# Optimization experiments

Hardware: AMD Instinct MI355X
Metric: run time of the kernel (lower is better)

Reference implementation:

```python
import jax, jax.numpy as jnp
import numpy as np

D = 512      # d_model
H = 8        # nhead
HD = D // H  # head dim
L = 8        # axis-0 length (torch seq dim, batch_first=False)
S = 128      # axis-1 length (torch batch dim; relation-tensor axis)
NL = 3       # encoder layers
EPS = 1e-5


def setup_inputs() -> dict:
    key = jax.random.key(0)
    ks = jax.random.split(key, 16)
    w = lambda k, shape: jax.random.normal(k, shape, jnp.float32) * 0.02
    return {
        "x": jax.random.normal(ks[0], (L, S, D), jnp.float32),
        # stacked per-layer transformer params (leading dim = NL)
        "attn_in_w": w(ks[1], (NL, 3 * D, D)), "attn_in_b": jnp.zeros((NL, 3 * D), jnp.float32),
        "attn_out_w": w(ks[2], (NL, D, D)),    "attn_out_b": jnp.zeros((NL, D), jnp.float32),
        "ln1_w": jnp.ones((NL, D), jnp.float32), "ln1_b": jnp.zeros((NL, D), jnp.float32),
        "ln2_w": jnp.ones((NL, D), jnp.float32), "ln2_b": jnp.zeros((NL, D), jnp.float32),
        "ff1_w": w(ks[3], (NL, 4 * D, D)), "ff1_b": jnp.zeros((NL, 4 * D), jnp.float32),
        "ff2_w": w(ks[4], (NL, D, 4 * D)), "ff2_b": jnp.zeros((NL, D), jnp.float32),
        "fln_w": jnp.ones((D,), jnp.float32), "fln_b": jnp.zeros((D,), jnp.float32),
        # 4 projection MLPs stacked: 0=sub, 1=obj, 2=verb_sub, 3=verb_obj
        "mlp_w0": w(ks[5], (4, D, D)), "mlp_b0": jnp.zeros((4, D), jnp.float32),
        "mlp_w1": w(ks[6], (4, D, D)), "mlp_b1": jnp.zeros((4, D), jnp.float32),
        "mlp_w2": w(ks[7], (4, D, D)), "mlp_b2": jnp.zeros((4, D), jnp.float32),
    }


def _ln(x, w, b):
    m = jnp.mean(x, axis=-1, keepdims=True)
    v = jnp.mean(jnp.square(x - m), axis=-1, keepdims=True)
    return (x - m) * jax.lax.rsqrt(v + EPS) * w + b


def _mha(x, in_w, in_b, out_w, out_b):
    # x: (L, B, D); attention over axis 0 (torch batch_first=False semantics)
    l, b, _ = x.shape
    qkv = x @ in_w.T + in_b                      # (L, B, 3D)
    q, k, v = jnp.split(qkv, 3, axis=-1)
    q = q.reshape(l, b, H, HD)
    k = k.reshape(l, b, H, HD)
    v = v.reshape(l, b, H, HD)
    scores = jnp.einsum("lbhd,mbhd->bhlm", q, k) / jnp.sqrt(jnp.float32(HD))
    attn = jax.nn.softmax(scores, axis=-1)
    o = jnp.einsum("bhlm,mbhd->lbhd", attn, v).reshape(l, b, D)
    return o @ out_w.T + out_b


def _mlp(x, w0, b0, w1, b1, w2, b2):
    h = jax.nn.relu(x @ w0.T + b0)
    h = jax.nn.relu(h @ w1.T + b1)
    return h @ w2.T + b2


def _forward(x, attn_in_w, attn_in_b, attn_out_w, attn_out_b,
             ln1_w, ln1_b, ln2_w, ln2_b, ff1_w, ff1_b, ff2_w, ff2_b,
             fln_w, fln_b, mlp_w0, mlp_b0, mlp_w1, mlp_b1, mlp_w2, mlp_b2):
    # TransformerEncoder (post-norm, relu, no dropout at eval)
    h = x
    for i in range(NL):
        h = _ln(h + _mha(h, attn_in_w[i], attn_in_b[i], attn_out_w[i], attn_out_b[i]),
                ln1_w[i], ln1_b[i])
        ff = jax.nn.relu(h @ ff1_w[i].T + ff1_b[i]) @ ff2_w[i].T + ff2_b[i]
        h = _ln(h + ff, ln2_w[i], ln2_b[i])
    h = _ln(h, fln_w, fln_b)  # final encoder norm

    sub = _mlp(h, mlp_w0[0], mlp_b0[0], mlp_w1[0], mlp_b1[0], mlp_w2[0], mlp_b2[0])
    obj = _mlp(h, mlp_w0[1], mlp_b0[1], mlp_w1[1], mlp_b1[1], mlp_w2[1], mlp_b2[1])
    vsub = _mlp(h, mlp_w0[2], mlp_b0[2], mlp_w1[2], mlp_b1[2], mlp_w2[2], mlp_b2[2])
    vobj = _mlp(h, mlp_w0[3], mlp_b0[3], mlp_w1[3], mlp_b1[3], mlp_w2[3], mlp_b2[3])

    # sub.unsqueeze(1) * vsub.unsqueeze(2): (B0, S, S, D)
    sub4 = sub[:, None, :, :] * vsub[:, :, None, :]
    obj4 = obj[:, None, :, :] * vobj[:, :, None, :]
    # p_x = sub4 @ obj4.transpose(-2, -1): (B0, S, S, S)
    return jnp.einsum("bijd,bikd->bijk", sub4, obj4)


def reference(x, attn_in_w, attn_in_b, attn_out_w, attn_out_b,
              ln1_w, ln1_b, ln2_w, ln2_b, ff1_w, ff1_b, ff2_w, ff2_b,
              fln_w, fln_b, mlp_w0, mlp_b0, mlp_w1, mlp_b1, mlp_w2, mlp_b2):
    return _forward(x, attn_in_w, attn_in_b, attn_out_w, attn_out_b,
                    ln1_w, ln1_b, ln2_w, ln2_b, ff1_w, ff1_b, ff2_w, ff2_b,
                    fln_w, fln_b, mlp_w0, mlp_b0, mlp_w1, mlp_b1, mlp_w2, mlp_b2)
```

## Files before the change

kernel.cpp:

```cpp
#include <hip/hip_runtime.h>
#include <hip/hip_bf16.h>

#define DEV __device__ __forceinline__

typedef __attribute__((ext_vector_type(8))) short bf16x8;
typedef __attribute__((ext_vector_type(8))) unsigned short u16x8;
typedef __attribute__((ext_vector_type(4))) float f32x4;

DEV unsigned short f2bf(float f) {
  return __builtin_bit_cast(unsigned short, __float2bfloat16(f));
}
DEV float bf2f(unsigned short h) { return __uint_as_float(((unsigned int)h) << 16); }

DEV int swz(int row, int byteoff) { return row * 128 + (byteoff ^ ((row & 7) << 4)); }

struct CvtJobs { const float* s[8]; unsigned short* d[8]; int n[8]; };
__global__ void cvtw_kernel(CvtJobs J) {
  const int seg = blockIdx.y;
  const float* __restrict__ src = J.s[seg];
  unsigned short* __restrict__ dst = J.d[seg];
  const int n = J.n[seg];
  long i = ((long)blockIdx.x * blockDim.x + threadIdx.x) * 8;
  long stride = (long)gridDim.x * blockDim.x * 8;
  for (; i < n; i += stride) {
    f32x4 a = *(const f32x4*)(src + i);
    f32x4 b = *(const f32x4*)(src + i + 4);
    u16x8 o;
    o[0] = f2bf(a[0]); o[1] = f2bf(a[1]); o[2] = f2bf(a[2]); o[3] = f2bf(a[3]);
    o[4] = f2bf(b[0]); o[5] = f2bf(b[1]); o[6] = f2bf(b[2]); o[7] = f2bf(b[3]);
    *(u16x8*)(dst + i) = o;
  }
}

template <int BM, int BN, int ALN, int RES, int RLN, int ACT, int STATS, int OUTF32, int OUTBF>
__global__ __launch_bounds__(256) void gemm2_kernel(
    const unsigned short* __restrict__ Xb, const float* __restrict__ Xf,
    const float* __restrict__ sA, const float* __restrict__ gA, const float* __restrict__ bA,
    const unsigned short* __restrict__ W, const float* __restrict__ bias,
    const float* __restrict__ resf, const float* __restrict__ sR,
    const float* __restrict__ gR, const float* __restrict__ bR,
    float* __restrict__ Yf, unsigned short* __restrict__ Ybf, float* __restrict__ stats,
    int M, int N, int K, long xbs, long wbs, long bbs, long ybs) {
  constexpr int CA = BM / 32, CB = BN / 32;
  constexpr int ABY = BM * 64 * 2, BBY = BN * 64 * 2;
  constexpr int MI = BM / 32, NI = BN / 32;
  __shared__ __align__(16) char Asb[2 * ABY];
  __shared__ __align__(16) char Bsb[2 * BBY];
  const int t = threadIdx.x;
  const int bn = blockIdx.x, bm = blockIdx.y, bz = blockIdx.z;
  const int lane = t & 63, wv = t >> 6, wr = wv >> 1, wc = wv & 1;

  int rowA[CA], slotA[CA], rowB[CB], slotB[CB];
#pragma unroll
  for (int c = 0; c < CA; ++c) { int id = c * 256 + t; rowA[c] = id >> 3; slotA[c] = id & 7; }
#pragma unroll
  for (int c = 0; c < CB; ++c) { int id = c * 256 + t; rowB[c] = id >> 3; slotB[c] = id & 7; }

  float mA[CA], iA[CA];
  if (ALN) {
#pragma unroll
    for (int c = 0; c < CA; ++c) {
      const int gm = bm * BM + rowA[c];
      const float s = sA[2 * gm], q = sA[2 * gm + 1];
      mA[c] = s * (1.f / 512.f);
      iA[c] = rsqrtf(q * (1.f / 512.f) - mA[c] * mA[c] + 1e-5f);
    }
  }

  f32x4 acc[MI][NI];
#pragma unroll
  for (int mi = 0; mi < MI; ++mi)
#pragma unroll
    for (int ni = 0; ni < NI; ++ni) acc[mi][ni] = f32x4{0.f, 0.f, 0.f, 0.f};

  u16x8 ra[CA], rb[CB];
  f32x4 raf[CA][2];
  auto load = [&](int kt) {
#pragma unroll
    for (int c = 0; c < CA; ++c) {
      if (ALN) {
        const float* p = Xf + (long)(bm * BM + rowA[c]) * K + kt + slotA[c] * 8;
        raf[c][0] = *(const f32x4*)p;
        raf[c][1] = *(const f32x4*)(p + 4);
      } else {
        ra[c] = *(const u16x8*)(Xb + (long)bz * xbs + (long)(bm * BM + rowA[c]) * K + kt + slotA[c] * 8);
      }
    }
#pragma unroll
    for (int c = 0; c < CB; ++c)
      rb[c] = *(const u16x8*)(W + (long)bz * wbs + (long)(bn * BN + rowB[c]) * K + kt + slotB[c] * 8);
  };
  auto store = [&](int cur, int kt) {
#pragma unroll
    for (int c = 0; c < CA; ++c) {
      if (ALN) {
        const int col = kt + slotA[c] * 8;
        f32x4 g0 = *(const f32x4*)(gA + col), g1 = *(const f32x4*)(gA + col + 4);
        f32x4 b0 = *(const f32x4*)(bA + col), b1 = *(const f32x4*)(bA + col + 4);
        u16x8 o;
#pragma unroll
        for (int j = 0; j < 4; ++j) o[j] = f2bf((raf[c][0][j] - mA[c]) * iA[c] * g0[j] + b0[j]);
#pragma unroll
        for (int j = 0; j < 4; ++j) o[4 + j] = f2bf((raf[c][1][j] - mA[c]) * iA[c] * g1[j] + b1[j]);
        *(u16x8*)(Asb + cur * ABY + swz(rowA[c], slotA[c] * 16)) = o;
      } else {
        *(u16x8*)(Asb + cur * ABY + swz(rowA[c], slotA[c] * 16)) = ra[c];
      }
    }
#pragma unroll
    for (int c = 0; c < CB; ++c)
      *(u16x8*)(Bsb + cur * BBY + swz(rowB[c], slotB[c] * 16)) = rb[c];
  };

  const int NT = K >> 6;
  load(0);
  store(0, 0);
  load(64);
  __syncthreads();
  for (int ki = 0; ki < NT; ++ki) {
    const int cur = ki & 1;
    if (ki + 1 < NT) store(cur ^ 1, (ki + 1) << 6);
    if (ki + 2 < NT) load((ki + 2) << 6);
#pragma unroll
    for (int kk = 0; kk < 2; ++kk) {
      const int kb = kk * 64 + ((lane >> 4) << 4);
      bf16x8 af[MI], bfv[NI];
#pragma unroll
      for (int mi = 0; mi < MI; ++mi)
        af[mi] = *(const bf16x8*)(Asb + cur * ABY + swz(wr * (BM / 2) + mi * 16 + (lane & 15), kb));
#pragma unroll
      for (int ni = 0; ni < NI; ++ni)
        bfv[ni] = *(const bf16x8*)(Bsb + cur * BBY + swz(wc * (BN / 2) + ni * 16 + (lane & 15), kb));
#pragma unroll
      for (int mi = 0; mi < MI; ++mi)
#pragma unroll
        for (int ni = 0; ni < NI; ++ni)
          acc[mi][ni] = __builtin_amdgcn_mfma_f32_16x16x32_bf16(af[mi], bfv[ni], acc[mi][ni], 0, 0, 0);
    }
    __syncthreads();
  }

#pragma unroll
  for (int mi = 0; mi < MI; ++mi) {
#pragma unroll
    for (int rr = 0; rr < 4; ++rr) {
      const int gm = bm * BM + wr * (BM / 2) + mi * 16 + ((lane >> 4) << 2) + rr;
      float mR, iR;
      if (RES && RLN) {
        const float s = sR[2 * gm], q = sR[2 * gm + 1];
        mR = s * (1.f / 512.f);
        iR = rsqrtf(q * (1.f / 512.f) - mR * mR + 1e-5f);
      }
      float srow = 0.f, qrow = 0.f;
#pragma unroll
      for (int ni = 0; ni < NI; ++ni) {
        const int gn = bn * BN + wc * (BN / 2) + ni * 16 + (lane & 15);
        float v = acc[mi][ni][rr] + bias[(long)bz * bbs + gn];
        if (RES) {
          float r = resf[(long)gm * 512 + gn];
          if (RLN) r = (r - mR) * iR * gR[gn] + bR[gn];
          v += r;
        }
        if (ACT) v = fmaxf(v, 0.f);
        if (STATS) { srow += v; qrow += v * v; }
        const long o = (long)bz * ybs + (long)gm * N + gn;
        if (OUTF32) Yf[o] = v;
        if (OUTBF) Ybf[o] = f2bf(v);
      }
      if (STATS) {
#pragma unroll
        for (int msk = 1; msk < 16; msk <<= 1) {
          srow += __shfl_xor(srow, msk, 64);
          qrow += __shfl_xor(qrow, msk, 64);
        }
        if ((lane & 15) == 0) {
          atomicAdd(&stats[2 * gm], srow);
          atomicAdd(&stats[2 * gm + 1], qrow);
        }
      }
    }
  }
}

__global__ __launch_bounds__(256) void attn_kernel(const unsigned short* __restrict__ qkv,
                                                   unsigned short* __restrict__ o) {
  __shared__ float P[512];
  const int s = blockIdx.x;
  const int t = threadIdx.x;
#pragma unroll
  for (int rep = 0; rep < 2; ++rep) {
    const int idx = t + rep * 256;
    const int h = idx >> 6, l = (idx >> 3) & 7, m = idx & 7;
    const unsigned short* qp = qkv + (long)(l * 128 + s) * 1536 + h * 64;
    const unsigned short* kp = qkv + (long)(m * 128 + s) * 1536 + 512 + h * 64;
    float acc = 0.f;
#pragma unroll
    for (int c = 0; c < 64; c += 8) {
      u16x8 q8 = *(const u16x8*)(qp + c);
      u16x8 k8 = *(const u16x8*)(kp + c);
#pragma unroll
      for (int j = 0; j < 8; ++j) acc += bf2f(q8[j]) * bf2f(k8[j]);
    }
    P[idx] = acc * 0.125f;
  }
  __syncthreads();
  if (t < 64) {
    const int base = t * 8;
    float mx = -1e30f;
#pragma unroll
    for (int m = 0; m < 8; ++m) mx = fmaxf(mx, P[base + m]);
    float e[8], sum = 0.f;
#pragma unroll
    for (int m = 0; m < 8; ++m) { e[m] = expf(P[base + m] - mx); sum += e[m]; }
    const float inv = 1.f / sum;
#pragma unroll
    for (int m = 0; m < 8; ++m) P[base + m] = e[m] * inv;
  }
  __syncthreads();
#pragma unroll
  for (int rep = 0; rep < 16; ++rep) {
    const int idx = t + rep * 256;
    const int d = idx & 63, h = (idx >> 6) & 7, l = idx >> 9;
    float acc = 0.f;
#pragma unroll
    for (int m = 0; m < 8; ++m)
      acc += P[h * 64 + l * 8 + m] * bf2f(qkv[(long)(m * 128 + s) * 1536 + 1024 + h * 64 + d]);
    o[(long)(l * 128 + s) * 512 + h * 64 + d] = f2bf(acc);
  }
}

__global__ __launch_bounds__(256) void lastln_kernel(const float* __restrict__ t2,
                                                     const float* __restrict__ S,
                                                     const float* __restrict__ g2,
                                                     const float* __restrict__ b2,
                                                     const float* __restrict__ gf,
                                                     const float* __restrict__ bf_,
                                                     unsigned short* __restrict__ out) {
  const int t = threadIdx.x, lane = t & 63, wv = t >> 6;
  const int row = blockIdx.x * 4 + wv;
  const float* p = t2 + (long)row * 512 + lane * 8;
  f32x4 a = *(const f32x4*)p;
  f32x4 c = *(const f32x4*)(p + 4);
  const float s0 = S[2 * row], q0 = S[2 * row + 1];
  const float m1 = s0 * (1.f / 512.f);
  const float i1 = rsqrtf(q0 * (1.f / 512.f) - m1 * m1 + 1e-5f);
  float v[8];
  const float* g2p = g2 + lane * 8;
  const float* b2p = b2 + lane * 8;
#pragma unroll
  for (int j = 0; j < 4; ++j) v[j] = (a[j] - m1) * i1 * g2p[j] + b2p[j];
#pragma unroll
  for (int j = 0; j < 4; ++j) v[4 + j] = (c[j] - m1) * i1 * g2p[4 + j] + b2p[4 + j];
  float s = 0.f, q = 0.f;
#pragma unroll
  for (int j = 0; j < 8; ++j) { s += v[j]; q += v[j] * v[j]; }
#pragma unroll
  for (int msk = 32; msk; msk >>= 1) { s += __shfl_xor(s, msk, 64); q += __shfl_xor(q, msk, 64); }
  const float m2 = s * (1.f / 512.f);
  const float i2 = rsqrtf(q * (1.f / 512.f) - m2 * m2 + 1e-5f);
  const float* gfp = gf + lane * 8;
  const float* bfp = bf_ + lane * 8;
  u16x8 o;
#pragma unroll
  for (int j = 0; j < 8; ++j) o[j] = f2bf((v[j] - m2) * i2 * gfp[j] + bfp[j]);
  *(u16x8*)(out + (long)row * 512 + lane * 8) = o;
}

__global__ __launch_bounds__(256) void phasec_kernel(const float* __restrict__ subp,
                                                     const unsigned short* __restrict__ objbf,
                                                     const float* __restrict__ vsub,
                                                     const float* __restrict__ vobj,
                                                     float* __restrict__ out) {
  constexpr int ABY = 128 * 64 * 2;
  __shared__ __align__(16) char SMEM[67584];
  char* Asb = SMEM;
  char* Bsb = SMEM + 2 * ABY;
  float* Wl = (float*)(SMEM + 4 * ABY);
  const int t = threadIdx.x;
  const int i = blockIdx.x, b = blockIdx.y;
  const long base_bi = ((long)b * 128 + i) * 512;
  for (int d = t; d < 512; d += 256) Wl[d] = vsub[base_bi + d] * vobj[base_bi + d];

  const int lane = t & 63, wv = t >> 6;
  const int wr = wv >> 1, wc = wv & 1;
  f32x4 acc[4][4] = {};

  int row[4], slot[4];
#pragma unroll
  for (int c = 0; c < 4; ++c) { int id = c * 256 + t; row[c] = id >> 3; slot[c] = id & 7; }

  f32x4 fa[4][2];
  u16x8 rb[4];
  auto load = [&](int kt) {
#pragma unroll
    for (int c = 0; c < 4; ++c) {
      const long g = ((long)b * 128 + row[c]) * 512 + kt + slot[c] * 8;
      fa[c][0] = *(const f32x4*)(subp + g);
      fa[c][1] = *(const f32x4*)(subp + g + 4);
      rb[c] = *(const u16x8*)(objbf + g);
    }
  };
  auto store = [&](int cur, int ktd) {
#pragma unroll
    for (int c = 0; c < 4; ++c) {
      const float* wp = Wl + ktd + slot[c] * 8;
      f32x4 w0 = *(const f32x4*)wp;
      f32x4 w1 = *(const f32x4*)(wp + 4);
      u16x8 oa;
      oa[0] = f2bf(fa[c][0][0] * w0[0]); oa[1] = f2bf(fa[c][0][1] * w0[1]);
      oa[2] = f2bf(fa[c][0][2] * w0[2]); oa[3] = f2bf(fa[c][0][3] * w0[3]);
      oa[4] = f2bf(fa[c][1][0] * w1[0]); oa[5] = f2bf(fa[c][1][1] * w1[1]);
      oa[6] = f2bf(fa[c][1][2] * w1[2]); oa[7] = f2bf(fa[c][1][3] * w1[3]);
      *(u16x8*)(Asb + cur * ABY + swz(row[c], slot[c] * 16)) = oa;
      *(u16x8*)(Bsb + cur * ABY + swz(row[c], slot[c] * 16)) = rb[c];
    }
  };

  __syncthreads();
  load(0);
  store(0, 0);
  load(64);
  __syncthreads();
  for (int ki = 0; ki < 8; ++ki) {
    const int cur = ki & 1;
    if (ki + 1 < 8) store(cur ^ 1, (ki + 1) * 64);
    if (ki + 2 < 8) load((ki + 2) * 64);
#pragma unroll
    for (int kk = 0; kk < 2; ++kk) {
      const int kb = kk * 64 + ((lane >> 4) << 4);
      bf16x8 af[4], bfv[4];
#pragma unroll
      for (int mi = 0; mi < 4; ++mi)
        af[mi] = *(const bf16x8*)(Asb + cur * ABY + swz(wr * 64 + mi * 16 + (lane & 15), kb));
#pragma unroll
      for (int ni = 0; ni < 4; ++ni)
        bfv[ni] = *(const bf16x8*)(Bsb + cur * ABY + swz(wc * 64 + ni * 16 + (lane & 15), kb));
#pragma unroll
      for (int mi = 0; mi < 4; ++mi)
#pragma unroll
        for (int ni = 0; ni < 4; ++ni)
          acc[mi][ni] = __builtin_amdgcn_mfma_f32_16x16x32_bf16(af[mi], bfv[ni], acc[mi][ni], 0, 0, 0);
    }
    __syncthreads();
  }
  float* C = (float*)SMEM;
#pragma unroll
  for (int mi = 0; mi < 4; ++mi)
#pragma unroll
    for (int rr = 0; rr < 4; ++rr) {
      const int j = wr * 64 + mi * 16 + ((lane >> 4) << 2) + rr;
      float* crow = C + j * 132 + wc * 64 + (lane & 15);
#pragma unroll
      for (int ni = 0; ni < 4; ++ni) crow[ni * 16] = acc[mi][ni][rr];
    }
  __syncthreads();
  float* ob = out + ((long)b * 128 + i) * 128 * 128;
  const int cc = (t & 31) * 4, jb = (t >> 5) * 16;
#pragma unroll
  for (int q = 0; q < 16; ++q) {
    const int j = jb + q;
    f32x4 v = *(const f32x4*)(C + j * 132 + cc);
    *(f32x4*)(ob + (long)j * 128 + cc) = v;
  }
}

extern "C" void kernel_launch(void* const* d_in, const int* in_sizes, int n_in, void* d_out,
                              int out_size, void* d_ws, size_t ws_size, hipStream_t stream) {
  const float* x          = (const float*)d_in[0];
  const float* attn_in_w  = (const float*)d_in[1];
  const float* attn_in_b  = (const float*)d_in[2];
  const float* attn_out_w = (const float*)d_in[3];
  const float* attn_out_b = (const float*)d_in[4];
  const float* ln1_w = (const float*)d_in[5];
  const float* ln1_b = (const float*)d_in[6];
  const float* ln2_w = (const float*)d_in[7];
  const float* ln2_b = (const float*)d_in[8];
  const float* ff1_w = (const float*)d_in[9];
  const float* ff1_b = (const float*)d_in[10];
  const float* ff2_w = (const float*)d_in[11];
  const float* ff2_b = (const float*)d_in[12];
  const float* fln_w = (const float*)d_in[13];
  const float* fln_b = (const float*)d_in[14];
  const float* mlp_w0 = (const float*)d_in[15];
  const float* mlp_b0 = (const float*)d_in[16];
  const float* mlp_w1 = (const float*)d_in[17];
  const float* mlp_b1 = (const float*)d_in[18];
  const float* mlp_w2 = (const float*)d_in[19];
  const float* mlp_b2 = (const float*)d_in[20];
  float* out = (float*)d_out;
  (void)in_sizes; (void)n_in; (void)out_size; (void)ws_size;

  char* ws = (char*)d_ws;
  size_t off = 0;
  auto alloc = [&](size_t bytes) -> void* {
    void* p = (void*)(ws + off);
    off += (bytes + 255) & ~(size_t)255;
    return p;
  };
  float* stats        = (float*)alloc((size_t)6 * 1024 * 2 * 4);
  unsigned short* wq  = (unsigned short*)alloc((size_t)3 * 1536 * 512 * 2);
  unsigned short* wo  = (unsigned short*)alloc((size_t)3 * 512 * 512 * 2);
  unsigned short* wf1 = (unsigned short*)alloc((size_t)3 * 2048 * 512 * 2);
  unsigned short* wf2 = (unsigned short*)alloc((size_t)3 * 512 * 2048 * 2);
  unsigned short* wm0 = (unsigned short*)alloc((size_t)4 * 512 * 512 * 2);
  unsigned short* wm1 = (unsigned short*)alloc((size_t)4 * 512 * 512 * 2);
  unsigned short* wm2 = (unsigned short*)alloc((size_t)4 * 512 * 512 * 2);
  unsigned short* hbf0 = (unsigned short*)alloc((size_t)1024 * 512 * 2);
  unsigned short* t1  = (unsigned short*)alloc((size_t)1024 * 2048 * 2);
  unsigned short* ao  = (unsigned short*)alloc((size_t)1024 * 512 * 2);
  float* t2a          = (float*)alloc((size_t)1024 * 512 * 4);
  float* t2b          = (float*)alloc((size_t)1024 * 512 * 4);
  unsigned short* hbfH = (unsigned short*)alloc((size_t)1024 * 512 * 2);
  unsigned short* z1  = (unsigned short*)alloc((size_t)4 * 1024 * 512 * 2);
  unsigned short* z2  = (unsigned short*)alloc((size_t)4 * 1024 * 512 * 2);
  float* hf4          = (float*)alloc((size_t)4 * 1024 * 512 * 4);
  unsigned short* hb4 = (unsigned short*)alloc((size_t)4 * 1024 * 512 * 2);

  hipMemsetAsync(stats, 0, (size_t)6 * 1024 * 2 * 4, stream);

  CvtJobs J;
  J.s[0] = attn_in_w;  J.d[0] = wq;  J.n[0] = 3 * 1536 * 512;
  J.s[1] = attn_out_w; J.d[1] = wo;  J.n[1] = 3 * 512 * 512;
  J.s[2] = ff1_w;      J.d[2] = wf1; J.n[2] = 3 * 2048 * 512;
  J.s[3] = ff2_w;      J.d[3] = wf2; J.n[3] = 3 * 512 * 2048;
  J.s[4] = mlp_w0;     J.d[4] = wm0; J.n[4] = 4 * 512 * 512;
  J.s[5] = mlp_w1;     J.d[5] = wm1; J.n[5] = 4 * 512 * 512;
  J.s[6] = mlp_w2;     J.d[6] = wm2; J.n[6] = 4 * 512 * 512;
  J.s[7] = x;          J.d[7] = hbf0; J.n[7] = 1024 * 512;
  cvtw_kernel<<<dim3(512, 8), 256, 0, stream>>>(J);

  for (int L = 0; L < 3; ++L) {
    float* Sout = stats + (2 * L) * 2048;
    float* Sff  = stats + (2 * L + 1) * 2048;
    const float* Sprev = stats + (2 * L - 1) * 2048;
    if (L == 0)
      gemm2_kernel<64, 128, 0, 0, 0, 0, 0, 0, 1><<<dim3(12, 16), 256, 0, stream>>>(
          hbf0, nullptr, nullptr, nullptr, nullptr, wq, attn_in_b, nullptr, nullptr, nullptr,
          nullptr, nullptr, t1, nullptr, 1024, 1536, 512, 0, 0, 0, 0);
    else
      gemm2_kernel<64, 128, 1, 0, 0, 0, 0, 0, 1><<<dim3(12, 16), 256, 0, stream>>>(
          nullptr, t2b, Sprev, ln2_w + (L - 1) * 512, ln2_b + (L - 1) * 512,
          wq + (long)L * 1536 * 512, attn_in_b + L * 1536, nullptr, nullptr, nullptr,
          nullptr, nullptr, t1, nullptr, 1024, 1536, 512, 0, 0, 0, 0);
    attn_kernel<<<128, 256, 0, stream>>>(t1, ao);
    if (L == 0)
      gemm2_kernel<32, 64, 0, 1, 0, 0, 1, 1, 0><<<dim3(8, 32), 256, 0, stream>>>(
          ao, nullptr, nullptr, nullptr, nullptr, wo, attn_out_b, x, nullptr, nullptr, nullptr,
          t2a, nullptr, Sout, 1024, 512, 512, 0, 0, 0, 0);
    else
      gemm2_kernel<32, 64, 0, 1, 1, 0, 1, 1, 0><<<dim3(8, 32), 256, 0, stream>>>(
          ao, nullptr, nullptr, nullptr, nullptr, wo + (long)L * 512 * 512, attn_out_b + L * 512,
          t2b, Sprev, ln2_w + (L - 1) * 512, ln2_b + (L - 1) * 512,
          t2a, nullptr, Sout, 1024, 512, 512, 0, 0, 0, 0);
    gemm2_kernel<64, 128, 1, 0, 0, 1, 0, 0, 1><<<dim3(16, 16), 256, 0, stream>>>(
        nullptr, t2a, Sout, ln1_w + L * 512, ln1_b + L * 512,
        wf1 + (long)L * 2048 * 512, ff1_b + L * 2048, nullptr, nullptr, nullptr, nullptr,
        nullptr, t1, nullptr, 1024, 2048, 512, 0, 0, 0, 0);
    gemm2_kernel<32, 64, 0, 1, 1, 0, 1, 1, 0><<<dim3(8, 32), 256, 0, stream>>>(
        t1, nullptr, nullptr, nullptr, nullptr, wf2 + (long)L * 512 * 2048, ff2_b + L * 512,
        t2a, Sout, ln1_w + L * 512, ln1_b + L * 512,
        t2b, nullptr, Sff, 1024, 512, 2048, 0, 0, 0, 0);
  }
  lastln_kernel<<<256, 256, 0, stream>>>(t2b, stats + 5 * 2048, ln2_w + 2 * 512, ln2_b + 2 * 512,
                                         fln_w, fln_b, hbfH);
  gemm2_kernel<64, 128, 0, 0, 0, 1, 0, 0, 1><<<dim3(4, 16, 4), 256, 0, stream>>>(
      hbfH, nullptr, nullptr, nullptr, nullptr, wm0, mlp_b0, nullptr, nullptr, nullptr, nullptr,
      nullptr, z1, nullptr, 1024, 512, 512, 0, 512 * 512, 512, 1024 * 512);
  gemm2_kernel<64, 128, 0, 0, 0, 1, 0, 0, 1><<<dim3(4, 16, 4), 256, 0, stream>>>(
      z1, nullptr, nullptr, nullptr, nullptr, wm1, mlp_b1, nullptr, nullptr, nullptr, nullptr,
      nullptr, z2, nullptr, 1024, 512, 512, 1024 * 512, 512 * 512, 512, 1024 * 512);
  gemm2_kernel<64, 128, 0, 0, 0, 0, 0, 1, 1><<<dim3(4, 16, 4), 256, 0, stream>>>(
      z2, nullptr, nullptr, nullptr, nullptr, wm2, mlp_b2, nullptr, nullptr, nullptr, nullptr,
      hf4, hb4, nullptr, 1024, 512, 512, 1024 * 512, 512 * 512, 512, 1024 * 512);

  phasec_kernel<<<dim3(128, 8), 256, 0, stream>>>(
      hf4, hb4 + 1 * 1024 * 512, hf4 + 2L * 1024 * 512, hf4 + 3L * 1024 * 512, out);
}
```

Baseline: 388.8 us.

## Drop weight pre-conversion kernel and fuse attention with output projection

Removes the separate fp32-to-bf16 conversion pass over all weights and the input. GEMMs now load fp32 weights (and fp32 x in layer 0) and convert them while staging into shared memory. The attention kernel is merged with the output projection, residual add and LayerNorm statistics into one 512-thread kernel per sequence column. This saves a launch and a global round trip of the attention output, at the cost of reading fp32 weights in every GEMM tile and giving the fused kernel only 128 blocks with each block sweeping the full 512x512 output weight.

Measured after the change: 412.3 us. 6.1% more time.

```diff
diff --git a/kernel.cpp b/kernel.cpp
--- a/kernel.cpp
+++ b/kernel.cpp
@@ -14,29 +14,13 @@
 
 DEV int swz(int row, int byteoff) { return row * 128 + (byteoff ^ ((row & 7) << 4)); }
 
-struct CvtJobs { const float* s[8]; unsigned short* d[8]; int n[8]; };
-__global__ void cvtw_kernel(CvtJobs J) {
-  const int seg = blockIdx.y;
-  const float* __restrict__ src = J.s[seg];
-  unsigned short* __restrict__ dst = J.d[seg];
-  const int n = J.n[seg];
-  long i = ((long)blockIdx.x * blockDim.x + threadIdx.x) * 8;
-  long stride = (long)gridDim.x * blockDim.x * 8;
-  for (; i < n; i += stride) {
-    f32x4 a = *(const f32x4*)(src + i);
-    f32x4 b = *(const f32x4*)(src + i + 4);
-    u16x8 o;
-    o[0] = f2bf(a[0]); o[1] = f2bf(a[1]); o[2] = f2bf(a[2]); o[3] = f2bf(a[3]);
-    o[4] = f2bf(b[0]); o[5] = f2bf(b[1]); o[6] = f2bf(b[2]); o[7] = f2bf(b[3]);
-    *(u16x8*)(dst + i) = o;
-  }
-}
-
-template <int BM, int BN, int ALN, int RES, int RLN, int ACT, int STATS, int OUTF32, int OUTBF>
+template <int BM, int BN, int ALN, int AF32, int WF32, int RES, int RLN, int ACT, int STATS,
+          int OUTF32, int OUTBF>
 __global__ __launch_bounds__(256) void gemm2_kernel(
     const unsigned short* __restrict__ Xb, const float* __restrict__ Xf,
     const float* __restrict__ sA, const float* __restrict__ gA, const float* __restrict__ bA,
-    const unsigned short* __restrict__ W, const float* __restrict__ bias,
+    const unsigned short* __restrict__ Wb, const float* __restrict__ Wf,
+    const float* __restrict__ bias,
     const float* __restrict__ resf, const float* __restrict__ sR,
     const float* __restrict__ gR, const float* __restrict__ bR,
     float* __restrict__ Yf, unsigned short* __restrict__ Ybf, float* __restrict__ stats,
@@ -74,11 +58,11 @@
     for (int ni = 0; ni < NI; ++ni) acc[mi][ni] = f32x4{0.f, 0.f, 0.f, 0.f};
 
   u16x8 ra[CA], rb[CB];
-  f32x4 raf[CA][2];
+  f32x4 raf[CA][2], rbf[CB][2];
   auto load = [&](int kt) {
 #pragma unroll
     for (int c = 0; c < CA; ++c) {
-      if (ALN) {
+      if (ALN || AF32) {
         const float* p = Xf + (long)(bm * BM + rowA[c]) * K + kt + slotA[c] * 8;
         raf[c][0] = *(const f32x4*)p;
         raf[c][1] = *(const f32x4*)(p + 4);
@@ -87,29 +71,51 @@
       }
     }
 #pragma unroll
-    for (int c = 0; c < CB; ++c)
-      rb[c] = *(const u16x8*)(W + (long)bz * wbs + (long)(bn * BN + rowB[c]) * K + kt + slotB[c] * 8);
+    for (int c = 0; c < CB; ++c) {
+      if (WF32) {
+        const float* p = Wf + (long)bz * wbs + (long)(bn * BN + rowB[c]) * K + kt + slotB[c] * 8;
+        rbf[c][0] = *(const f32x4*)p;
+        rbf[c][1] = *(const f32x4*)(p + 4);
+      } else {
+        rb[c] = *(const u16x8*)(Wb + (long)bz * wbs + (long)(bn * BN + rowB[c]) * K + kt + slotB[c] * 8);
+      }
+    }
   };
   auto store = [&](int cur, int kt) {
 #pragma unroll
     for (int c = 0; c < CA; ++c) {
+      u16x8 o;
       if (ALN) {
         const int col = kt + slotA[c] * 8;
         f32x4 g0 = *(const f32x4*)(gA + col), g1 = *(const f32x4*)(gA + col + 4);
         f32x4 b0 = *(const f32x4*)(bA + col), b1 = *(const f32x4*)(bA + col + 4);
-        u16x8 o;
 #pragma unroll
         for (int j = 0; j < 4; ++j) o[j] = f2bf((raf[c][0][j] - mA[c]) * iA[c] * g0[j] + b0[j]);
 #pragma unroll
         for (int j = 0; j < 4; ++j) o[4 + j] = f2bf((raf[c][1][j] - mA[c]) * iA[c] * g1[j] + b1[j]);
-        *(u16x8*)(Asb + cur * ABY + swz(rowA[c], slotA[c] * 16)) = o;
+      } else if (AF32) {
+#pragma unroll
+        for (int j = 0; j < 4; ++j) o[j] = f2bf(raf[c][0][j]);
+#pragma unroll
+        for (int j = 0; j < 4; ++j) o[4 + j] = f2bf(raf[c][1][j]);
       } else {
-        *(u16x8*)(Asb + cur * ABY + swz(rowA[c], slotA[c] * 16)) = ra[c];
-      }
-    }
-#pragma unroll
-    for (int c = 0; c < CB; ++c)
-      *(u16x8*)(Bsb + cur * BBY + swz(rowB[c], slotB[c] * 16)) = rb[c];
+        o = ra[c];
+      }
+      *(u16x8*)(Asb + cur * ABY + swz(rowA[c], slotA[c] * 16)) = o;
+    }
+#pragma unroll
+    for (int c = 0; c < CB; ++c) {
+      u16x8 o;
+      if (WF32) {
+#pragma unroll
+        for (int j = 0; j < 4; ++j) o[j] = f2bf(rbf[c][0][j]);
+#pragma unroll
+        for (int j = 0; j < 4; ++j) o[4 + j] = f2bf(rbf[c][1][j]);
+      } else {
+        o = rb[c];
+      }
+      *(u16x8*)(Bsb + cur * BBY + swz(rowB[c], slotB[c] * 16)) = o;
+    }
   };
 
   const int NT = K >> 6;
@@ -182,15 +188,50 @@
   }
 }
 
-__global__ __launch_bounds__(256) void attn_kernel(const unsigned short* __restrict__ qkv,
-                                                   unsigned short* __restrict__ o) {
+template <int RLN>
+__global__ __launch_bounds__(512) void attnop_kernel(
+    const unsigned short* __restrict__ qkv, const float* __restrict__ Wf,
+    const float* __restrict__ bias, const float* __restrict__ resf,
+    const float* __restrict__ sR, const float* __restrict__ gR, const float* __restrict__ bR,
+    float* __restrict__ t2a, float* __restrict__ stats) {
   __shared__ float P[512];
+  __shared__ float Sred[8][16][2];
+  __shared__ __align__(16) char As[16 * 1024];
+  __shared__ __align__(16) char Bs[2 * 128 * 128];
   const int s = blockIdx.x;
   const int t = threadIdx.x;
-#pragma unroll
-  for (int rep = 0; rep < 2; ++rep) {
-    const int idx = t + rep * 256;
-    const int h = idx >> 6, l = (idx >> 3) & 7, m = idx & 7;
+  const int lane = t & 63, w = t >> 6;
+
+  int rowB[2], slotB[2];
+#pragma unroll
+  for (int c = 0; c < 2; ++c) { int id = c * 512 + t; rowB[c] = id >> 3; slotB[c] = id & 7; }
+  f32x4 rbf[2][2];
+  auto loadB = [&](int tau) {
+    const int nb = (tau >> 3) * 128, kt = (tau & 7) * 64;
+#pragma unroll
+    for (int c = 0; c < 2; ++c) {
+      const float* p = Wf + (long)(nb + rowB[c]) * 512 + kt + slotB[c] * 8;
+      rbf[c][0] = *(const f32x4*)p;
+      rbf[c][1] = *(const f32x4*)(p + 4);
+    }
+  };
+  auto storeB = [&](int cur) {
+#pragma unroll
+    for (int c = 0; c < 2; ++c) {
+      u16x8 o;
+#pragma unroll
+      for (int j = 0; j < 4; ++j) o[j] = f2bf(rbf[c][0][j]);
+#pragma unroll
+      for (int j = 0; j < 4; ++j) o[4 + j] = f2bf(rbf[c][1][j]);
+      *(u16x8*)(Bs + cur * 16384 + swz(rowB[c], slotB[c] * 16)) = o;
+    }
+  };
+  loadB(0);
+
+  *(f32x4*)(As + 8 * 1024 + t * 16) = f32x4{0.f, 0.f, 0.f, 0.f};
+
+  {
+    const int h = t >> 6, l = (t >> 3) & 7, m = t & 7;
     const unsigned short* qp = qkv + (long)(l * 128 + s) * 1536 + h * 64;
     const unsigned short* kp = qkv + (long)(m * 128 + s) * 1536 + 512 + h * 64;
     float acc = 0.f;
@@ -201,7 +242,7 @@
 #pragma unroll
       for (int j = 0; j < 8; ++j) acc += bf2f(q8[j]) * bf2f(k8[j]);
     }
-    P[idx] = acc * 0.125f;
+    P[t] = acc * 0.125f;
   }
   __syncthreads();
   if (t < 64) {
@@ -217,15 +258,82 @@
     for (int m = 0; m < 8; ++m) P[base + m] = e[m] * inv;
   }
   __syncthreads();
-#pragma unroll
-  for (int rep = 0; rep < 16; ++rep) {
-    const int idx = t + rep * 256;
-    const int d = idx & 63, h = (idx >> 6) & 7, l = idx >> 9;
-    float acc = 0.f;
-#pragma unroll
-    for (int m = 0; m < 8; ++m)
-      acc += P[h * 64 + l * 8 + m] * bf2f(qkv[(long)(m * 128 + s) * 1536 + 1024 + h * 64 + d]);
-    o[(long)(l * 128 + s) * 512 + h * 64 + d] = f2bf(acc);
+  {
+    const int l = t >> 6, c0 = lane * 8, h = c0 >> 6;
+    float o[8] = {0.f, 0.f, 0.f, 0.f, 0.f, 0.f, 0.f, 0.f};
+#pragma unroll
+    for (int m = 0; m < 8; ++m) {
+      const float p = P[h * 64 + l * 8 + m];
+      u16x8 v8 = *(const u16x8*)(qkv + (long)(m * 128 + s) * 1536 + 1024 + c0);
+#pragma unroll
+      for (int j = 0; j < 8; ++j) o[j] += p * bf2f(v8[j]);
+    }
+    u16x8 pk;
+#pragma unroll
+    for (int j = 0; j < 8; ++j) pk[j] = f2bf(o[j]);
+    *(u16x8*)(As + l * 1024 + ((c0 * 2) ^ ((l & 7) << 4))) = pk;
+  }
+  __syncthreads();
+
+  f32x4 acc[4] = {};
+  storeB(0);
+  loadB(1);
+  __syncthreads();
+  for (int tau = 0; tau < 32; ++tau) {
+    const int cur = tau & 1;
+    if (tau + 1 < 32) storeB(cur ^ 1);
+    if (tau + 2 < 32) loadB(tau + 2);
+    const int nc = tau >> 3;
+#pragma unroll
+    for (int kk = 0; kk < 2; ++kk) {
+      const int arow = lane & 15;
+      const int kbyte = ((tau & 7) << 7) + (kk << 6) + ((lane >> 4) << 4);
+      bf16x8 af = *(const bf16x8*)(As + arow * 1024 + (kbyte ^ ((arow & 7) << 4)));
+      bf16x8 bv = *(const bf16x8*)(Bs + cur * 16384 +
+                                   swz(w * 16 + (lane & 15), (kk << 6) + ((lane >> 4) << 4)));
+      acc[nc] = __builtin_amdgcn_mfma_f32_16x16x32_bf16(af, bv, acc[nc], 0, 0, 0);
+    }
+    __syncthreads();
+  }
+
+#pragma unroll
+  for (int rr = 0; rr < 4; ++rr) {
+    const int l = ((lane >> 4) << 2) + rr;
+    if (l < 8) {
+      const int g = l * 128 + s;
+      float mR, iR;
+      if (RLN) {
+        const float sv = sR[2 * g], qv = sR[2 * g + 1];
+        mR = sv * (1.f / 512.f);
+        iR = rsqrtf(qv * (1.f / 512.f) - mR * mR + 1e-5f);
+      }
+      float sr = 0.f, qr = 0.f;
+#pragma unroll
+      for (int nc = 0; nc < 4; ++nc) {
+        const int n = nc * 128 + w * 16 + (lane & 15);
+        float v = acc[nc][rr] + bias[n];
+        float r = resf[(long)g * 512 + n];
+        if (RLN) r = (r - mR) * iR * gR[n] + bR[n];
+        v += r;
+        sr += v; qr += v * v;
+        t2a[(long)g * 512 + n] = v;
+      }
+#pragma unroll
+      for (int msk = 1; msk < 16; msk <<= 1) {
+        sr += __shfl_xor(sr, msk, 64);
+        qr += __shfl_xor(qr, msk, 64);
+      }
+      if ((lane & 15) == 0) { Sred[w][l][0] = sr; Sred[w][l][1] = qr; }
+    }
+  }
+  __syncthreads();
+  if (t < 8) {
+    float S = 0.f, Q = 0.f;
+#pragma unroll
+    for (int ww = 0; ww < 8; ++ww) { S += Sred[ww][t][0]; Q += Sred[ww][t][1]; }
+    const int g = t * 128 + s;
+    stats[2 * g] = S;
+    stats[2 * g + 1] = Q;
   }
 }
 
@@ -397,81 +505,65 @@
     off += (bytes + 255) & ~(size_t)255;
     return p;
   };
-  float* stats        = (float*)alloc((size_t)6 * 1024 * 2 * 4);
-  unsigned short* wq  = (unsigned short*)alloc((size_t)3 * 1536 * 512 * 2);
-  unsigned short* wo  = (unsigned short*)alloc((size_t)3 * 512 * 512 * 2);
-  unsigned short* wf1 = (unsigned short*)alloc((size_t)3 * 2048 * 512 * 2);
-  unsigned short* wf2 = (unsigned short*)alloc((size_t)3 * 512 * 2048 * 2);
-  unsigned short* wm0 = (unsigned short*)alloc((size_t)4 * 512 * 512 * 2);
-  unsigned short* wm1 = (unsigned short*)alloc((size_t)4 * 512 * 512 * 2);
-  unsigned short* wm2 = (unsigned short*)alloc((size_t)4 * 512 * 512 * 2);
-  unsigned short* hbf0 = (unsigned short*)alloc((size_t)1024 * 512 * 2);
-  unsigned short* t1  = (unsigned short*)alloc((size_t)1024 * 2048 * 2);
-  unsigned short* ao  = (unsigned short*)alloc((size_t)1024 * 512 * 2);
-  float* t2a          = (float*)alloc((size_t)1024 * 512 * 4);
-  float* t2b          = (float*)alloc((size_t)1024 * 512 * 4);
+  float* stats         = (float*)alloc((size_t)6 * 1024 * 2 * 4);
+  unsigned short* t1   = (unsigned short*)alloc((size_t)1024 * 2048 * 2);
+  float* t2a           = (float*)alloc((size_t)1024 * 512 * 4);
+  float* t2b           = (float*)alloc((size_t)1024 * 512 * 4);
   unsigned short* hbfH = (unsigned short*)alloc((size_t)1024 * 512 * 2);
-  unsigned short* z1  = (unsigned short*)alloc((size_t)4 * 1024 * 512 * 2);
-  unsigned short* z2  = (unsigned short*)alloc((size_t)4 * 1024 * 512 * 2);
-  float* hf4          = (float*)alloc((size_t)4 * 1024 * 512 * 4);
-  unsigned short* hb4 = (unsigned short*)alloc((size_t)4 * 1024 * 512 * 2);
+  unsigned short* z1   = (unsigned short*)alloc((size_t)4 * 1024 * 512 * 2);
+  unsigned short* z2   = (unsigned short*)alloc((size_t)4 * 1024 * 512 * 2);
+  float* hf4           = (float*)alloc((size_t)4 * 1024 * 512 * 4);
+  unsigned short* hb4  = (unsigned short*)alloc((size_t)4 * 1024 * 512 * 2);
 
   hipMemsetAsync(stats, 0, (size_t)6 * 1024 * 2 * 4, stream);
-
-  CvtJobs J;
-  J.s[0] = attn_in_w;  J.d[0] = wq;  J.n[0] = 3 * 1536 * 512;
-  J.s[1] = attn_out_w; J.d[1] = wo;  J.n[1] = 3 * 512 * 512;
-  J.s[2] = ff1_w;      J.d[2] = wf1; J.n[2] = 3 * 2048 * 512;
-  J.s[3] = ff2_w;      J.d[3] = wf2; J.n[3] = 3 * 512 * 2048;
-  J.s[4] = mlp_w0;     J.d[4] = wm0; J.n[4] = 4 * 512 * 512;
-  J.s[5] = mlp_w1;     J.d[5] = wm1; J.n[5] = 4 * 512 * 512;
-  J.s[6] = mlp_w2;     J.d[6] = wm2; J.n[6] = 4 * 512 * 512;
-  J.s[7] = x;          J.d[7] = hbf0; J.n[7] = 1024 * 512;
-  cvtw_kernel<<<dim3(512, 8), 256, 0, stream>>>(J);
 
   for (int L = 0; L < 3; ++L) {
     float* Sout = stats + (2 * L) * 2048;
     float* Sff  = stats + (2 * L + 1) * 2048;
     const float* Sprev = stats + (2 * L - 1) * 2048;
     if (L == 0)
-      gemm2_kernel<64, 128, 0, 0, 0, 0, 0, 0, 1><<<dim3(12, 16), 256, 0, stream>>>(
-          hbf0, nullptr, nullptr, nullptr, nullptr, wq, attn_in_b, nullptr, nullptr, nullptr,
-          nullptr, nullptr, t1, nullptr, 1024, 1536, 512, 0, 0, 0, 0);
+      gemm2_kernel<64, 128, 0, 1, 1, 0, 0, 0, 0, 0, 1><<<dim3(12, 16), 256, 0, stream>>>(
+          nullptr, x, nullptr, nullptr, nullptr, nullptr, attn_in_w, attn_in_b,
+          nullptr, nullptr, nullptr, nullptr, nullptr, t1, nullptr,
+          1024, 1536, 512, 0, 0, 0, 0);
     else
-      gemm2_kernel<64, 128, 1, 0, 0, 0, 0, 0, 1><<<dim3(12, 16), 256, 0, stream>>>(
+      gemm2_kernel<64, 128, 1, 0, 1, 0, 0, 0, 0, 0, 1><<<dim3(12, 16), 256, 0, stream>>>(
           nullptr, t2b, Sprev, ln2_w + (L - 1) * 512, ln2_b + (L - 1) * 512,
-          wq + (long)L * 1536 * 512, attn_in_b + L * 1536, nullptr, nullptr, nullptr,
-          nullptr, nullptr, t1, nullptr, 1024, 1536, 512, 0, 0, 0, 0);
-    attn_kernel<<<128, 256, 0, stream>>>(t1, ao);
+          nullptr, attn_in_w + (long)L * 1536 * 512, attn_in_b + L * 1536,
+          nullptr, nullptr, nullptr, nullptr, nullptr, t1, nullptr,
+          1024, 1536, 512, 0, 0, 0, 0);
     if (L == 0)
-      gemm2_kernel<32, 64, 0, 1, 0, 0, 1, 1, 0><<<dim3(8, 32), 256, 0, stream>>>(
-          ao, nullptr, nullptr, nullptr, nullptr, wo, attn_out_b, x, nullptr, nullptr, nullptr,
-          t2a, nullptr, Sout, 1024, 512, 512, 0, 0, 0, 0);
+      attnop_kernel<0><<<128, 512, 0, stream>>>(
+          t1, attn_out_w, attn_out_b, x, nullptr, nullptr, nullptr, t2a, Sout);
     else
-      gemm2_kernel<32, 64, 0, 1, 1, 0, 1, 1, 0><<<dim3(8, 32), 256, 0, stream>>>(
-          ao, nullptr, nullptr, nullptr, nullptr, wo + (long)L * 512 * 512, attn_out_b + L * 512,
-          t2b, Sprev, ln2_w + (L - 1) * 512, ln2_b + (L - 1) * 512,
-          t2a, nullptr, Sout, 1024, 512, 512, 0, 0, 0, 0);
-    gemm2_kernel<64, 128, 1, 0, 0, 1, 0, 0, 1><<<dim3(16, 16), 256, 0, stream>>>(
+      attnop_kernel<1><<<128, 512, 0, stream>>>(
+          t1, attn_out_w + (long)L * 512 * 512, attn_out_b + L * 512, t2b,
+          Sprev, ln2_w + (L - 1) * 512, ln2_b + (L - 1) * 512, t2a, Sout);
+    gemm2_kernel<64, 128, 1, 0, 1, 0, 0, 1, 0, 0, 1><<<dim3(16, 16), 256, 0, stream>>>(
         nullptr, t2a, Sout, ln1_w + L * 512, ln1_b + L * 512,
-        wf1 + (long)L * 2048 * 512, ff1_b + L * 2048, nullptr, nullptr, nullptr, nullptr,
-        nullptr, t1, nullptr, 1024, 2048, 512, 0, 0, 0, 0);
-    gemm2_kernel<32, 64, 0, 1, 1, 0, 1, 1, 0><<<dim3(8, 32), 256, 0, stream>>>(
-        t1, nullptr, nullptr, nullptr, nullptr, wf2 + (long)L * 512 * 2048, ff2_b + L * 512,
+        nullptr, ff1_w + (long)L * 2048 * 512, ff1_b + L * 2048,
+        nullptr, nullptr, nullptr, nullptr, nullptr, t1, nullptr,
+        1024, 2048, 512, 0, 0, 0, 0);
+    gemm2_kernel<32, 64, 0, 0, 1, 1, 1, 0, 1, 1, 0><<<dim3(8, 32), 256, 0, stream>>>(
+        t1, nullptr, nullptr, nullptr, nullptr,
+        nullptr, ff2_w + (long)L * 512 * 2048, ff2_b + L * 512,
         t2a, Sout, ln1_w + L * 512, ln1_b + L * 512,
         t2b, nullptr, Sff, 1024, 512, 2048, 0, 0, 0, 0);
   }
   lastln_kernel<<<256, 256, 0, stream>>>(t2b, stats + 5 * 2048, ln2_w + 2 * 512, ln2_b + 2 * 512,
                                          fln_w, fln_b, hbfH);
-  gemm2_kernel<64, 128, 0, 0, 0, 1, 0, 0, 1><<<dim3(4, 16, 4), 256, 0, stream>>>(
-      hbfH, nullptr, nullptr, nullptr, nullptr, wm0, mlp_b0, nullptr, nullptr, nullptr, nullptr,
-      nullptr, z1, nullptr, 1024, 512, 512, 0, 512 * 512, 512, 1024 * 512);
-  gemm2_kernel<64, 128, 0, 0, 0, 1, 0, 0, 1><<<dim3(4, 16, 4), 256, 0, stream>>>(
-      z1, nullptr, nullptr, nullptr, nullptr, wm1, mlp_b1, nullptr, nullptr, nullptr, nullptr,
-      nullptr, z2, nullptr, 1024, 512, 512, 1024 * 512, 512 * 512, 512, 1024 * 512);
-  gemm2_kernel<64, 128, 0, 0, 0, 0, 0, 1, 1><<<dim3(4, 16, 4), 256, 0, stream>>>(
-      z2, nullptr, nullptr, nullptr, nullptr, wm2, mlp_b2, nullptr, nullptr, nullptr, nullptr,
-      hf4, hb4, nullptr, 1024, 512, 512, 1024 * 512, 512 * 512, 512, 1024 * 512);
+  gemm2_kernel<64, 128, 0, 0, 1, 0, 0, 1, 0, 0, 1><<<dim3(4, 16, 4), 256, 0, stream>>>(
+      hbfH, nullptr, nullptr, nullptr, nullptr, nullptr, mlp_w0, mlp_b0,
+      nullptr, nullptr, nullptr, nullptr, nullptr, z1, nullptr,
+      1024, 512, 512, 0, 512 * 512, 512, 1024 * 512);
+  gemm2_kernel<64, 128, 0, 0, 1, 0, 0, 1, 0, 0, 1><<<dim3(4, 16, 4), 256, 0, stream>>>(
+      z1, nullptr, nullptr, nullptr, nullptr, nullptr, mlp_w1, mlp_b1,
+      nullptr, nullptr, nullptr, nullptr, nullptr, z2, nullptr,
+      1024, 512, 512, 1024 * 512, 512 * 512, 512, 1024 * 512);
+  gemm2_kernel<64, 128, 0, 0, 1, 0, 0, 0, 0, 1, 1><<<dim3(4, 16, 4), 256, 0, stream>>>(
+      z2, nullptr, nullptr, nullptr, nullptr, nullptr, mlp_w2, mlp_b2,
+      nullptr, nullptr, nullptr, nullptr, hf4, hb4, nullptr,
+      1024, 512, 512, 1024 * 512, 512 * 512, 512, 1024 * 512);
 
   phasec_kernel<<<dim3(128, 8), 256, 0, stream>>>(
       hf4, hb4 + 1 * 1024 * 512, hf4 + 2L * 1024 * 512, hf4 + 3L * 1024 * 512, out);
```
